# Optimization experiments

Hardware: AMD Instinct MI355X
Metric: run time of the kernel (lower is better)

## Reference

```python
import jax, jax.numpy as jnp
import numpy as np

B, S, D = 32, 512, 768
HEADS = 12
CLUSTER = 5
INDEX = 256


def setup_inputs() -> dict:
    key = jax.random.key(0)
    kx, ka = jax.random.split(key)
    x = jax.random.normal(kx, (B, S, D), dtype=jnp.float32)
    atten = jax.random.uniform(ka, (B * HEADS, S, S), dtype=jnp.float32)
    return {"x": x, "atten": atten}


def reference(x, atten):
    b, s, d = x.shape
    # mean attention over heads: [B, S, S]
    avg_atten = atten.reshape(b, HEADS, s, s).mean(axis=1)
    # attended-by score per token: column sums minus diagonal
    attended_by = avg_atten.sum(axis=1) - jnp.diagonal(avg_atten, axis1=1, axis2=2)
    attended_by = attended_by[:, 1:]  # drop CLS column -> [B, S-1]
    # full descending sort (top_k with k = S-1)
    _, idx = jax.lax.top_k(attended_by, s - 1)
    # top tokens (shift +1 back to original positions), prepend CLS (=0), ascending order
    top_idx = jnp.sort(idx[:, : INDEX - 1 - CLUSTER] + 1, axis=1)
    cls = jnp.zeros((b, 1), dtype=top_idx.dtype)
    head_idx = jnp.concatenate([cls, top_idx], axis=1)  # 0 < all top_idx, so already sorted
    extract = jnp.take_along_axis(x, head_idx[:, :, None], axis=1)  # [B, INDEX-5, D]
    # tail tokens: softmax-weighted, pooled into CLUSTER clusters
    tail_idx = jnp.sort(idx[:, INDEX - CLUSTER :], axis=1)  # [B, T]
    tail_vals = jax.nn.softmax(jnp.take_along_axis(attended_by, tail_idx, axis=1), axis=1)
    tail_tokens = jnp.take_along_axis(x, (tail_idx + 1)[:, :, None], axis=1) * tail_vals[:, :, None]
    T = tail_tokens.shape[1]
    pad = CLUSTER - T % CLUSTER  # TF pads a full group when T % CLUSTER == 0
    tail_padded = jnp.pad(tail_tokens, ((0, 0), (0, pad), (0, 0)))
    clusters = tail_padded.reshape(b, CLUSTER, -1, d).mean(axis=2)  # [B, 5, D]
    return jnp.concatenate([extract, clusters], axis=1)  # [B, INDEX, D]
```

## Files before the change

kernel.cpp:

```cpp
#include <hip/hip_runtime.h>

#define NB 32
#define NS 512
#define ND 768
#define NHEADS 12
#define NTOK 511
#define NHEAD 250
#define NTAIL 260
#define CSIZE 53
#define NPART (NB * NHEADS * 4)
#define HEADB 1024

typedef float f4v __attribute__((ext_vector_type(4)));

__global__ __launch_bounds__(256) void colsum_kernel(const float* __restrict__ atten,
                                                     double* __restrict__ partials) {
    int blk   = blockIdx.x;
    int chunk = blk & 3;
    int tid   = threadIdx.x;
    int wave  = tid >> 6, lane = tid & 63;
    const float* base = atten + ((size_t)(blk >> 2)) * NS * NS;

    double a0=0,a1=0,a2=0,a3=0,a4=0,a5=0,a6=0,a7=0;
    #pragma unroll 8
    for (int i = 0; i < 32; ++i) {
        int r = chunk * 128 + wave + 4 * i;
        const float* row = base + (size_t)r * NS;
        f4v v0 = __builtin_nontemporal_load((const f4v*)(row + 4 * lane));
        f4v v1 = __builtin_nontemporal_load((const f4v*)(row + 256 + 4 * lane));
        if (chunk < 2) {
            int d = r - 4 * lane;
            if (d >= 0 && d < 4) {
                switch (d) {
                    case 0: v0.x = 0.f; break;
                    case 1: v0.y = 0.f; break;
                    case 2: v0.z = 0.f; break;
                    default: v0.w = 0.f; break;
                }
            }
        } else {
            int d = (r - 256) - 4 * lane;
            if (d >= 0 && d < 4) {
                switch (d) {
                    case 0: v1.x = 0.f; break;
                    case 1: v1.y = 0.f; break;
                    case 2: v1.z = 0.f; break;
                    default: v1.w = 0.f; break;
                }
            }
        }
        a0 += (double)v0.x; a1 += (double)v0.y; a2 += (double)v0.z; a3 += (double)v0.w;
        a4 += (double)v1.x; a5 += (double)v1.y; a6 += (double)v1.z; a7 += (double)v1.w;
    }

    __shared__ double sh[4 * NS];
    {
        double* d0 = sh + wave * NS + 4 * lane;
        d0[0]=a0; d0[1]=a1; d0[2]=a2; d0[3]=a3;
        double* d1 = sh + wave * NS + 256 + 4 * lane;
        d1[0]=a4; d1[1]=a5; d1[2]=a6; d1[3]=a7;
    }
    __syncthreads();
    for (int c = tid; c < NS; c += 256) {
        double s = sh[c] + sh[NS + c] + sh[2 * NS + c] + sh[3 * NS + c];
        partials[(size_t)blk * NS + c] = s;
    }
}

__global__ __launch_bounds__(512) void rank_kernel(const double* __restrict__ partials,
                                                   int* __restrict__ head_tok,
                                                   int* __restrict__ tail_tok,
                                                   float* __restrict__ tail_w) {
    int b = blockIdx.x;
    int t = threadIdx.x;
    int lane = t & 63, wave = t >> 6;

    __shared__ unsigned int hist[256];
    __shared__ unsigned int gts[8], eqs[8], hs[8], ts[8];
    __shared__ double dred[8];
    __shared__ unsigned long long s_K;
    __shared__ unsigned int s_R, s_byte, s_above;

    bool valid = t < NTOK;
    double val = 0.0;
    unsigned long long key = 0ull;
    if (valid) {
        const double* pp = partials + (size_t)b * 48 * NS + (t + 1);
        double s = 0;
        #pragma unroll 8
        for (int p = 0; p < 48; ++p) s += pp[(size_t)p * NS];
        val = s * (1.0 / 12.0);
        long long bits = __double_as_longlong(val);
        key = (bits >= 0) ? ((unsigned long long)bits | 0x8000000000000000ull)
                          : ~((unsigned long long)bits);
    }
    if (t == 0) { s_R = NHEAD + 1; s_K = 0ull; }
    __syncthreads();

    for (int pass = 7; pass >= 0; --pass) {
        if (t < 256) hist[t] = 0u;
        __syncthreads();
        if (valid) {
            bool cand = (pass == 7) ||
                ((key >> ((pass + 1) * 8)) == (s_K >> ((pass + 1) * 8)));
            if (cand) atomicAdd(&hist[(unsigned)((key >> (pass * 8)) & 0xFF)], 1u);
        }
        __syncthreads();
        if (wave == 0) {
            unsigned c0 = hist[4*lane+0], c1 = hist[4*lane+1];
            unsigned c2 = hist[4*lane+2], c3 = hist[4*lane+3];
            unsigned x = c0 + c1 + c2 + c3;
            #pragma unroll
            for (int off = 1; off < 64; off <<= 1) {
                unsigned n = __shfl_up(x, off);
                if (lane >= off) x += n;
            }
            unsigned tot = __shfl(x, 63);
            unsigned aboveLane = tot - x;
            unsigned R = s_R;
            unsigned a3 = aboveLane, a2 = a3 + c3, a1 = a2 + c2, a0 = a1 + c1;
            if (a3 < R && R <= a3 + c3) { s_byte = 4*lane+3; s_above = a3; }
            if (a2 < R && R <= a2 + c2) { s_byte = 4*lane+2; s_above = a2; }
            if (a1 < R && R <= a1 + c1) { s_byte = 4*lane+1; s_above = a1; }
            if (a0 < R && R <= a0 + c0) { s_byte = 4*lane+0; s_above = a0; }
        }
        __syncthreads();
        if (t == 0) {
            s_R -= s_above;
            s_K |= ((unsigned long long)s_byte) << (pass * 8);
        }
        __syncthreads();
    }
    unsigned long long K = s_K;

    bool gt = valid && (key > K);
    bool eq = valid && (key == K);
    unsigned long long mgt = __ballot(gt);
    unsigned long long meq = __ballot(eq);
    if (lane == 0) { gts[wave] = __popcll(mgt); eqs[wave] = __popcll(meq); }
    __syncthreads();
    unsigned cntGt = 0;
    #pragma unroll
    for (int w2 = 0; w2 < 8; ++w2) cntGt += gts[w2];
    unsigned eqBefore = __popcll(meq & ((1ull << lane) - 1ull));
    for (int w2 = 0; w2 < wave; ++w2) eqBefore += eqs[w2];
    unsigned rankEq = cntGt + eqBefore;
    bool isHead = gt || (eq && rankEq < NHEAD);
    bool isTail = valid && !gt && !(eq && rankEq <= NHEAD);

    unsigned long long mh = __ballot(isHead);
    unsigned long long mt = __ballot(isTail);
    if (lane == 0) { hs[wave] = __popcll(mh); ts[wave] = __popcll(mt); }
    __syncthreads();
    unsigned hslot = __popcll(mh & ((1ull << lane) - 1ull));
    unsigned tslot = __popcll(mt & ((1ull << lane) - 1ull));
    for (int w2 = 0; w2 < wave; ++w2) { hslot += hs[w2]; tslot += ts[w2]; }

    double tv = isTail ? val : -1.0e300;
    #pragma unroll
    for (int off = 32; off; off >>= 1) tv = fmax(tv, __shfl_xor(tv, off));
    if (lane == 0) dred[wave] = tv;
    __syncthreads();
    double m = dred[0];
    #pragma unroll
    for (int w2 = 1; w2 < 8; ++w2) m = fmax(m, dred[w2]);
    double e = isTail ? exp(val - m) : 0.0;
    double se = e;
    #pragma unroll
    for (int off = 32; off; off >>= 1) se += __shfl_xor(se, off);
    __syncthreads();
    if (lane == 0) dred[wave] = se;
    __syncthreads();
    double ssum = 0;
    #pragma unroll
    for (int w2 = 0; w2 < 8; ++w2) ssum += dred[w2];

    if (t == 0) head_tok[b * 256] = 0;
    if (isHead) head_tok[b * 256 + 1 + hslot] = t + 1;
    if (isTail) {
        tail_tok[b * 320 + tslot] = t + 1;
        tail_w [b * 320 + tslot] = (float)(e / ssum);
    }
}

__global__ __launch_bounds__(256) void gather_kernel(const float* __restrict__ x,
                                                     const int* __restrict__ head_tok,
                                                     const int* __restrict__ tail_tok,
                                                     const float* __restrict__ tail_w,
                                                     float* __restrict__ out) {
    int tid = threadIdx.x;
    if (blockIdx.x < HEADB) {
        const int TOTAL = NB * 251 * 192;
        for (int f = blockIdx.x * 256 + tid; f < TOTAL; f += HEADB * 256) {
            int rowIdx = f / 192;
            int c4 = (f - rowIdx * 192) * 4;
            int b = rowIdx / 251;
            int p = rowIdx - b * 251;
            int tok = head_tok[b * 256 + p];
            f4v vv = *(const f4v*)(x + ((size_t)(b * NS + tok)) * ND + c4);
            __builtin_nontemporal_store(vv,
                (f4v*)(out + ((size_t)(b * 256 + p)) * ND + c4));
        }
    } else {
        int cb = blockIdx.x - HEADB;
        int b = cb / 5, c = cb - b * 5;
        int t0 = c * CSIZE;
        int cnt = NTAIL - t0 < CSIZE ? NTAIL - t0 : CSIZE;
        __shared__ float wsh[CSIZE];
        __shared__ int   tsh[CSIZE];
        if (tid < cnt) {
            wsh[tid] = tail_w [b * 320 + t0 + tid];
            tsh[tid] = tail_tok[b * 320 + t0 + tid];
        }
        __syncthreads();
        if (tid < 192) {
            double s0 = 0, s1 = 0, s2 = 0, s3 = 0;
            #pragma unroll 4
            for (int k = 0; k < cnt; ++k) {
                float w = wsh[k];
                const f4v v = *(const f4v*)(x + ((size_t)(b * NS + tsh[k])) * ND + 4 * tid);
                s0 += (double)w * (double)v.x;
                s1 += (double)w * (double)v.y;
                s2 += (double)w * (double)v.z;
                s3 += (double)w * (double)v.w;
            }
            const double inv = 1.0 / (double)CSIZE;
            f4v r;
            r.x = (float)(s0 * inv); r.y = (float)(s1 * inv);
            r.z = (float)(s2 * inv); r.w = (float)(s3 * inv);
            __builtin_nontemporal_store(r,
                (f4v*)(out + ((size_t)(b * 256 + NHEAD + 1 + c)) * ND + 4 * tid));
        }
    }
}

extern "C" void kernel_launch(void* const* d_in, const int* in_sizes, int n_in,
                              void* d_out, int out_size, void* d_ws, size_t ws_size,
                              hipStream_t stream) {
    const float* x     = (const float*)d_in[0];
    const float* atten = (const float*)d_in[1];
    float* out = (float*)d_out;

    double* partials = (double*)d_ws;
    int*    head_tok = (int*)   ((char*)d_ws + 6291456);
    int*    tail_tok = (int*)   ((char*)d_ws + 6291456 + 32768);
    float*  tail_w   = (float*) ((char*)d_ws + 6291456 + 32768 + 40960);

    hipLaunchKernelGGL(colsum_kernel, dim3(NPART),        dim3(256), 0, stream, atten, partials);
    hipLaunchKernelGGL(rank_kernel,   dim3(NB),           dim3(512), 0, stream, partials,
                       head_tok, tail_tok, tail_w);
    hipLaunchKernelGGL(gather_kernel, dim3(HEADB + NB*5), dim3(256), 0, stream, x,
                       head_tok, tail_tok, tail_w, out);
}
```

Baseline: 98.28 us.

## Fuse column-sum and rank kernels via last-block-done atomic counter

```diff
diff --git a/kernel.cpp b/kernel.cpp
--- a/kernel.cpp
+++ b/kernel.cpp
@@ -8,27 +8,35 @@
 #define NHEAD 250
 #define NTAIL 260
 #define CSIZE 53
-#define NPART (NB * NHEADS * 4)
+#define K1B (NB * NHEADS * 2)
+#define BPB (NHEADS * 2)
 #define HEADB 1024
 
 typedef float f4v __attribute__((ext_vector_type(4)));
 
-__global__ __launch_bounds__(256) void colsum_kernel(const float* __restrict__ atten,
-                                                     double* __restrict__ partials) {
+__global__ __launch_bounds__(512) void colsum_rank_kernel(
+        const float* __restrict__ atten,
+        double* __restrict__ partials,
+        unsigned int* __restrict__ cnt,
+        int* __restrict__ head_tok,
+        int* __restrict__ tail_tok,
+        float* __restrict__ tail_w) {
     int blk   = blockIdx.x;
-    int chunk = blk & 3;
-    int tid   = threadIdx.x;
-    int wave  = tid >> 6, lane = tid & 63;
-    const float* base = atten + ((size_t)(blk >> 2)) * NS * NS;
+    int chunk = blk & 1;
+    int bh    = blk >> 1;
+    int b     = bh / NHEADS;
+    int t     = threadIdx.x;
+    int wave  = t >> 6, lane = t & 63;
+    const float* base = atten + (size_t)bh * NS * NS;
 
     double a0=0,a1=0,a2=0,a3=0,a4=0,a5=0,a6=0,a7=0;
     #pragma unroll 8
     for (int i = 0; i < 32; ++i) {
-        int r = chunk * 128 + wave + 4 * i;
+        int r = chunk * 256 + wave + 8 * i;
         const float* row = base + (size_t)r * NS;
         f4v v0 = __builtin_nontemporal_load((const f4v*)(row + 4 * lane));
         f4v v1 = __builtin_nontemporal_load((const f4v*)(row + 256 + 4 * lane));
-        if (chunk < 2) {
+        if (chunk == 0) {
             int d = r - 4 * lane;
             if (d >= 0 && d < 4) {
                 switch (d) {
@@ -53,7 +61,7 @@
         a4 += (double)v1.x; a5 += (double)v1.y; a6 += (double)v1.z; a7 += (double)v1.w;
     }
 
-    __shared__ double sh[4 * NS];
+    __shared__ double sh[8 * NS];
     {
         double* d0 = sh + wave * NS + 4 * lane;
         d0[0]=a0; d0[1]=a1; d0[2]=a2; d0[3]=a3;
@@ -61,20 +69,21 @@
         d1[0]=a4; d1[1]=a5; d1[2]=a6; d1[3]=a7;
     }
     __syncthreads();
-    for (int c = tid; c < NS; c += 256) {
-        double s = sh[c] + sh[NS + c] + sh[2 * NS + c] + sh[3 * NS + c];
-        partials[(size_t)blk * NS + c] = s;
-    }
-}
-
-__global__ __launch_bounds__(512) void rank_kernel(const double* __restrict__ partials,
-                                                   int* __restrict__ head_tok,
-                                                   int* __restrict__ tail_tok,
-                                                   float* __restrict__ tail_w) {
-    int b = blockIdx.x;
-    int t = threadIdx.x;
-    int lane = t & 63, wave = t >> 6;
-
+    {
+        double s = 0;
+        #pragma unroll
+        for (int w = 0; w < 8; ++w) s += sh[w * NS + t];
+        partials[(size_t)blk * NS + t] = s;
+    }
+    __threadfence();
+    __syncthreads();
+    __shared__ unsigned int sLast;
+    if (t == 0) sLast = (atomicAdd(&cnt[b], 1u) == BPB - 1) ? 1u : 0u;
+    __syncthreads();
+    if (!sLast) return;
+    __threadfence();
+
+    int lane2 = lane;
     __shared__ unsigned int hist[256];
     __shared__ unsigned int gts[8], eqs[8], hs[8], ts[8];
     __shared__ double dred[8];
@@ -85,10 +94,10 @@
     double val = 0.0;
     unsigned long long key = 0ull;
     if (valid) {
-        const double* pp = partials + (size_t)b * 48 * NS + (t + 1);
+        const double* pp = partials + (size_t)b * BPB * NS + (t + 1);
         double s = 0;
-        #pragma unroll 8
-        for (int p = 0; p < 48; ++p) s += pp[(size_t)p * NS];
+        #pragma unroll
+        for (int p = 0; p < BPB; ++p) s += pp[(size_t)p * NS];
         val = s * (1.0 / 12.0);
         long long bits = __double_as_longlong(val);
         key = (bits >= 0) ? ((unsigned long long)bits | 0x8000000000000000ull)
@@ -107,22 +116,22 @@
         }
         __syncthreads();
         if (wave == 0) {
-            unsigned c0 = hist[4*lane+0], c1 = hist[4*lane+1];
-            unsigned c2 = hist[4*lane+2], c3 = hist[4*lane+3];
+            unsigned c0 = hist[4*lane2+0], c1 = hist[4*lane2+1];
+            unsigned c2 = hist[4*lane2+2], c3 = hist[4*lane2+3];
             unsigned x = c0 + c1 + c2 + c3;
             #pragma unroll
             for (int off = 1; off < 64; off <<= 1) {
                 unsigned n = __shfl_up(x, off);
-                if (lane >= off) x += n;
+                if (lane2 >= off) x += n;
             }
             unsigned tot = __shfl(x, 63);
             unsigned aboveLane = tot - x;
             unsigned R = s_R;
-            unsigned a3 = aboveLane, a2 = a3 + c3, a1 = a2 + c2, a0 = a1 + c1;
-            if (a3 < R && R <= a3 + c3) { s_byte = 4*lane+3; s_above = a3; }
-            if (a2 < R && R <= a2 + c2) { s_byte = 4*lane+2; s_above = a2; }
-            if (a1 < R && R <= a1 + c1) { s_byte = 4*lane+1; s_above = a1; }
-            if (a0 < R && R <= a0 + c0) { s_byte = 4*lane+0; s_above = a0; }
+            unsigned a3c = aboveLane, a2c = a3c + c3, a1c = a2c + c2, a0c = a1c + c1;
+            if (a3c < R && R <= a3c + c3) { s_byte = 4*lane2+3; s_above = a3c; }
+            if (a2c < R && R <= a2c + c2) { s_byte = 4*lane2+2; s_above = a2c; }
+            if (a1c < R && R <= a1c + c1) { s_byte = 4*lane2+1; s_above = a1c; }
+            if (a0c < R && R <= a0c + c0) { s_byte = 4*lane2+0; s_above = a0c; }
         }
         __syncthreads();
         if (t == 0) {
@@ -137,12 +146,12 @@
     bool eq = valid && (key == K);
     unsigned long long mgt = __ballot(gt);
     unsigned long long meq = __ballot(eq);
-    if (lane == 0) { gts[wave] = __popcll(mgt); eqs[wave] = __popcll(meq); }
+    if (lane2 == 0) { gts[wave] = __popcll(mgt); eqs[wave] = __popcll(meq); }
     __syncthreads();
     unsigned cntGt = 0;
     #pragma unroll
     for (int w2 = 0; w2 < 8; ++w2) cntGt += gts[w2];
-    unsigned eqBefore = __popcll(meq & ((1ull << lane) - 1ull));
+    unsigned eqBefore = __popcll(meq & ((1ull << lane2) - 1ull));
     for (int w2 = 0; w2 < wave; ++w2) eqBefore += eqs[w2];
     unsigned rankEq = cntGt + eqBefore;
     bool isHead = gt || (eq && rankEq < NHEAD);
@@ -150,16 +159,16 @@
 
     unsigned long long mh = __ballot(isHead);
     unsigned long long mt = __ballot(isTail);
-    if (lane == 0) { hs[wave] = __popcll(mh); ts[wave] = __popcll(mt); }
-    __syncthreads();
-    unsigned hslot = __popcll(mh & ((1ull << lane) - 1ull));
-    unsigned tslot = __popcll(mt & ((1ull << lane) - 1ull));
+    if (lane2 == 0) { hs[wave] = __popcll(mh); ts[wave] = __popcll(mt); }
+    __syncthreads();
+    unsigned hslot = __popcll(mh & ((1ull << lane2) - 1ull));
+    unsigned tslot = __popcll(mt & ((1ull << lane2) - 1ull));
     for (int w2 = 0; w2 < wave; ++w2) { hslot += hs[w2]; tslot += ts[w2]; }
 
     double tv = isTail ? val : -1.0e300;
     #pragma unroll
     for (int off = 32; off; off >>= 1) tv = fmax(tv, __shfl_xor(tv, off));
-    if (lane == 0) dred[wave] = tv;
+    if (lane2 == 0) dred[wave] = tv;
     __syncthreads();
     double m = dred[0];
     #pragma unroll
@@ -169,7 +178,7 @@
     #pragma unroll
     for (int off = 32; off; off >>= 1) se += __shfl_xor(se, off);
     __syncthreads();
-    if (lane == 0) dred[wave] = se;
+    if (lane2 == 0) dred[wave] = se;
     __syncthreads();
     double ssum = 0;
     #pragma unroll
@@ -205,10 +214,10 @@
         int cb = blockIdx.x - HEADB;
         int b = cb / 5, c = cb - b * 5;
         int t0 = c * CSIZE;
-        int cnt = NTAIL - t0 < CSIZE ? NTAIL - t0 : CSIZE;
+        int cnt2 = NTAIL - t0 < CSIZE ? NTAIL - t0 : CSIZE;
         __shared__ float wsh[CSIZE];
         __shared__ int   tsh[CSIZE];
-        if (tid < cnt) {
+        if (tid < cnt2) {
             wsh[tid] = tail_w [b * 320 + t0 + tid];
             tsh[tid] = tail_tok[b * 320 + t0 + tid];
         }
@@ -216,7 +225,7 @@
         if (tid < 192) {
             double s0 = 0, s1 = 0, s2 = 0, s3 = 0;
             #pragma unroll 4
-            for (int k = 0; k < cnt; ++k) {
+            for (int k = 0; k < cnt2; ++k) {
                 float w = wsh[k];
                 const f4v v = *(const f4v*)(x + ((size_t)(b * NS + tsh[k])) * ND + 4 * tid);
                 s0 += (double)w * (double)v.x;
@@ -241,14 +250,16 @@
     const float* atten = (const float*)d_in[1];
     float* out = (float*)d_out;
 
-    double* partials = (double*)d_ws;
-    int*    head_tok = (int*)   ((char*)d_ws + 6291456);
-    int*    tail_tok = (int*)   ((char*)d_ws + 6291456 + 32768);
-    float*  tail_w   = (float*) ((char*)d_ws + 6291456 + 32768 + 40960);
-
-    hipLaunchKernelGGL(colsum_kernel, dim3(NPART),        dim3(256), 0, stream, atten, partials);
-    hipLaunchKernelGGL(rank_kernel,   dim3(NB),           dim3(512), 0, stream, partials,
-                       head_tok, tail_tok, tail_w);
-    hipLaunchKernelGGL(gather_kernel, dim3(HEADB + NB*5), dim3(256), 0, stream, x,
-                       head_tok, tail_tok, tail_w, out);
+    double*       partials = (double*)d_ws;
+    unsigned int* cnt      = (unsigned int*)((char*)d_ws + 3145728);
+    int*          head_tok = (int*)  ((char*)d_ws + 3145856);
+    int*          tail_tok = (int*)  ((char*)d_ws + 3145856 + 32768);
+    float*        tail_w   = (float*)((char*)d_ws + 3145856 + 32768 + 40960);
+
+    hipMemsetAsync(cnt, 0, 128, stream);
+
+    hipLaunchKernelGGL(colsum_rank_kernel, dim3(K1B), dim3(512), 0, stream,
+                       atten, partials, cnt, head_tok, tail_tok, tail_w);
+    hipLaunchKernelGGL(gather_kernel, dim3(HEADB + NB * 5), dim3(256), 0, stream,
+                       x, head_tok, tail_tok, tail_w, out);
 }
```

After: 317.3 us. 223% more time.
